# Optimization experiments

Measured on AMD Instinct MI355X. Metric: run time of the kernel, lower is better.

The kernel has to match this reference:

```python
import jax, jax.numpy as jnp
import numpy as np

B, C, H, W = 16, 64, 128, 128
BN_EPS = 1e-5


def setup_inputs() -> dict:
    key = jax.random.key(0)
    ks = jax.random.split(key, 8)
    inp = {
        "x1": jax.random.normal(ks[0], (B, C, H, W), dtype=jnp.float32),
        "x2": jax.random.normal(ks[1], (B, C, H, W), dtype=jnp.float32),
        "rssi1": jax.random.normal(ks[2], (B, C, H, W), dtype=jnp.float32),
        "rssi2": jax.random.normal(ks[3], (B, C, H, W), dtype=jnp.float32),
        # 1x1 conv weights == per-pixel channel matmul; trunc_normal(std=0.02) approximated by normal*0.02
        "q_w": jax.random.normal(ks[4], (C, C), dtype=jnp.float32) * 0.02,
        "q_b": jnp.zeros((C,), dtype=jnp.float32),
        "k_w": jax.random.normal(ks[5], (C, C), dtype=jnp.float32) * 0.02,
        "k_b": jnp.zeros((C,), dtype=jnp.float32),
        "v_w": jax.random.normal(ks[6], (C, C), dtype=jnp.float32) * 0.02,
        "v_b": jnp.zeros((C,), dtype=jnp.float32),
        "bn_gamma": jnp.ones((C,), dtype=jnp.float32),
        "bn_beta": jnp.zeros((C,), dtype=jnp.float32),
    }
    return inp


def _proj(w, b, x):
    # 1x1 Conv2d: contract channel dim
    return jnp.einsum('oc,bchw->bohw', w, x) + b[None, :, None, None]


def _branch(q_w, q_b, k_w, k_b, v_w, v_b, rssi, x):
    q = _proj(q_w, q_b, rssi)            # [B,C,H,W]
    k = _proj(k_w, k_b, x)               # [B,C,H,W]
    v = _proj(v_w, v_b, x)               # [B,C,H,W]
    scale = 1.0 / jnp.sqrt(jnp.asarray(k.shape[-2], dtype=q.dtype))
    # matmul over trailing dims: [B,C,H,W] @ [B,C,W,H] -> [B,C,H,H]
    score = jax.nn.softmax(jnp.einsum('bchw,bcgw->bchg', q, k) * scale, axis=-1)
    return jnp.einsum('bchg,bcgw->bchw', score, v)  # [B,C,H,W]


def reference(x1, x2, rssi1, rssi2, q_w, q_b, k_w, k_b, v_w, v_b, bn_gamma, bn_beta):
    csi1 = _branch(q_w, q_b, k_w, k_b, v_w, v_b, rssi1, x1)
    csi2 = _branch(q_w, q_b, k_w, k_b, v_w, v_b, rssi2, x2)
    fused = csi1 + csi2
    # BatchNorm2d (training mode -> batch statistics over B,H,W), then ReLU
    mean = jnp.mean(fused, axis=(0, 2, 3), keepdims=True)
    var = jnp.var(fused, axis=(0, 2, 3), keepdims=True)
    g = bn_gamma[None, :, None, None]
    b = bn_beta[None, :, None, None]
    normed = (fused - mean) * jax.lax.rsqrt(var + BN_EPS) * g + b
    return jax.nn.relu(normed)
```

## Files before the change

### kernel.cpp

```cpp
#include <hip/hip_runtime.h>

#define HW 16384
#define NE 16777216ull

typedef short bf16x8 __attribute__((ext_vector_type(8)));
typedef _Float16 f16x8 __attribute__((ext_vector_type(8)));
typedef float f32x4  __attribute__((ext_vector_type(4)));

__device__ __forceinline__ unsigned short f2bf(float f) {
    unsigned int u = __float_as_uint(f);
    unsigned int r = (u + 0x7FFFu + ((u >> 16) & 1u)) >> 16;
    return (unsigned short)r;
}
__device__ __forceinline__ float bf2f(unsigned short s) {
    return __uint_as_float(((unsigned int)s) << 16);
}

__global__ __launch_bounds__(128)
void zero_stats_kernel(float* __restrict__ stats) {
    stats[threadIdx.x] = 0.f;
}

__global__ __launch_bounds__(256)
void proj_mfma_kernel(const float* __restrict__ in,
                      const float* __restrict__ w1, const float* __restrict__ b1,
                      unsigned short* __restrict__ out1,
                      const float* __restrict__ w2, const float* __restrict__ b2,
                      unsigned short* __restrict__ out2) {
    __shared__ __align__(16) _Float16 xT[256 * 64];
    int tid = threadIdx.x;
    int pbase = blockIdx.x * 256;
    int b = pbase >> 14;
    int hw0 = pbase & 16383;
    const float* inb = in + (size_t)b * (64 * HW);

    {
        int n = tid;
        int swz = n & 7;
        const float* colp = inb + hw0 + n;
#pragma unroll
        for (int kc = 0; kc < 8; ++kc) {
            f16x8 ev;
#pragma unroll
            for (int j = 0; j < 8; ++j)
                ev[j] = (_Float16)colp[(kc * 8 + j) * HW];
            *reinterpret_cast<f16x8*>(&xT[n * 64 + ((kc ^ swz) * 8)]) = ev;
        }
    }

    int lane = tid & 63;
    int wv = tid >> 6;
    int quad = lane >> 4;
    int m16 = lane & 15;
    int mb = wv * 16;
    int sw = m16 & 7;
    int hasw2 = (w2 != nullptr);

    f16x8 a1[2], a2[2];
    float bias1[4], bias2[4];
#pragma unroll
    for (int ks = 0; ks < 2; ++ks) {
        const float* wr = w1 + (mb + m16) * 64 + (ks * 4 + quad) * 8;
        f16x8 ev;
#pragma unroll
        for (int j = 0; j < 8; ++j) ev[j] = (_Float16)wr[j];
        a1[ks] = ev;
    }
#pragma unroll
    for (int r = 0; r < 4; ++r) bias1[r] = b1[mb + quad * 4 + r];
    if (hasw2) {
#pragma unroll
        for (int ks = 0; ks < 2; ++ks) {
            const float* wr = w2 + (mb + m16) * 64 + (ks * 4 + quad) * 8;
            f16x8 ev;
#pragma unroll
            for (int j = 0; j < 8; ++j) ev[j] = (_Float16)wr[j];
            a2[ks] = ev;
        }
#pragma unroll
        for (int r = 0; r < 4; ++r) bias2[r] = b2[mb + quad * 4 + r];
    }
    __syncthreads();

    unsigned short* o1 = out1 + (size_t)b * (64 * HW);
    unsigned short* o2 = hasw2 ? (out2 + (size_t)b * (64 * HW)) : out1;

#pragma unroll
    for (int nt = 0; nt < 16; ++nt) {
        int row = nt * 16 + m16;
        f16x8 bF0 = *reinterpret_cast<const f16x8*>(&xT[row * 64 + ((quad ^ sw) * 8)]);
        f16x8 bF1 = *reinterpret_cast<const f16x8*>(&xT[row * 64 + (((4 + quad) ^ sw) * 8)]);
        f32x4 acc1 = {bias1[0], bias1[1], bias1[2], bias1[3]};
        acc1 = __builtin_amdgcn_mfma_f32_16x16x32_f16(a1[0], bF0, acc1, 0, 0, 0);
        acc1 = __builtin_amdgcn_mfma_f32_16x16x32_f16(a1[1], bF1, acc1, 0, 0, 0);
        int cbase = (mb + quad * 4) * HW + hw0 + nt * 16 + m16;
#pragma unroll
        for (int r = 0; r < 4; ++r)
            o1[cbase + r * HW] = f2bf(acc1[r]);
        if (hasw2) {
            f32x4 acc2 = {bias2[0], bias2[1], bias2[2], bias2[3]};
            acc2 = __builtin_amdgcn_mfma_f32_16x16x32_f16(a2[0], bF0, acc2, 0, 0, 0);
            acc2 = __builtin_amdgcn_mfma_f32_16x16x32_f16(a2[1], bF1, acc2, 0, 0, 0);
#pragma unroll
            for (int r = 0; r < 4; ++r)
                o2[cbase + r * HW] = f2bf(acc2[r]);
        }
    }
}

__global__ __launch_bounds__(512, 4)
void attn_kernel(const unsigned short* __restrict__ Q, const unsigned short* __restrict__ K,
                 const unsigned short* __restrict__ V, float* __restrict__ io,
                 float* __restrict__ stats, int accumulate) {
    __shared__ short bufA[16384];
    __shared__ short bufB[16384];
    int bc = blockIdx.x;
    size_t base = (size_t)bc * HW;
    int tid = threadIdx.x;
    int lane = tid & 63;
    int wv = tid >> 6;
    int quad = lane >> 4;
    int m16 = lane & 15;

    uint4 vreg[4];
    {
        int g0 = tid >> 4;
        int w0 = (tid & 15) * 8;
#pragma unroll
        for (int i = 0; i < 4; ++i)
            vreg[i] = *(const uint4*)(V + base + (size_t)(g0 + 32 * i) * 128 + w0);
    }

    {
        int r0 = tid >> 4;
        int c0 = tid & 15;
#pragma unroll
        for (int i = 0; i < 4; ++i) {
            int r = r0 + 32 * i;
            uint4 q = *(const uint4*)(Q + base + (size_t)r * 128 + c0 * 8);
            uint4 k = *(const uint4*)(K + base + (size_t)r * 128 + c0 * 8);
            int ch = c0 ^ (r & 7);
            *reinterpret_cast<uint4*>(&bufA[r * 128 + ch * 8]) = q;
            *reinterpret_cast<uint4*>(&bufB[r * 128 + ch * 8]) = k;
        }
    }
    __syncthreads();

    int rowA = wv * 16 + m16;
    int sw = m16 & 7;
    bf16x8 aF[4];
#pragma unroll
    for (int ks = 0; ks < 4; ++ks) {
        int ch = (ks * 4 + quad) ^ sw;
        aF[ks] = *reinterpret_cast<const bf16x8*>(&bufA[rowA * 128 + ch * 8]);
    }
    f32x4 sacc[8];
#pragma unroll
    for (int n = 0; n < 8; ++n) {
        f32x4 acc = {0.f, 0.f, 0.f, 0.f};
        int rowB = n * 16 + m16;
#pragma unroll
        for (int ks = 0; ks < 4; ++ks) {
            int ch = (ks * 4 + quad) ^ sw;
            bf16x8 bF = *reinterpret_cast<const bf16x8*>(&bufB[rowB * 128 + ch * 8]);
            acc = __builtin_amdgcn_mfma_f32_16x16x32_bf16(aF[ks], bF, acc, 0, 0, 0);
        }
        sacc[n] = acc;
    }

    const float scale = 0.08838834764831845f;
    float mx[4] = {-3.4e38f, -3.4e38f, -3.4e38f, -3.4e38f};
#pragma unroll
    for (int n = 0; n < 8; ++n)
#pragma unroll
        for (int r = 0; r < 4; ++r) {
            sacc[n][r] *= scale;
            mx[r] = fmaxf(mx[r], sacc[n][r]);
        }
#pragma unroll
    for (int mask = 8; mask >= 1; mask >>= 1)
#pragma unroll
        for (int r = 0; r < 4; ++r) mx[r] = fmaxf(mx[r], __shfl_xor(mx[r], mask));
    float sum[4] = {0.f, 0.f, 0.f, 0.f};
#pragma unroll
    for (int n = 0; n < 8; ++n)
#pragma unroll
        for (int r = 0; r < 4; ++r) {
            float e = __expf(sacc[n][r] - mx[r]);
            sacc[n][r] = e;
            sum[r] += e;
        }
#pragma unroll
    for (int mask = 8; mask >= 1; mask >>= 1)
#pragma unroll
        for (int r = 0; r < 4; ++r) sum[r] += __shfl_xor(sum[r], mask);
    float inv[4];
#pragma unroll
    for (int r = 0; r < 4; ++r) inv[r] = 1.0f / sum[r];

#pragma unroll
    for (int n = 0; n < 8; ++n)
#pragma unroll
        for (int r = 0; r < 4; ++r) {
            int row = wv * 16 + quad * 4 + r;
            int col = n * 16 + m16;
            int pos = row * 128 + (((col >> 3) ^ (row & 7)) * 8) + (col & 7);
            bufA[pos] = (short)f2bf(sacc[n][r] * inv[r]);
        }

    __syncthreads();

    {
        int g0 = tid >> 4;
        int w0 = (tid & 15) * 8;
#pragma unroll
        for (int i = 0; i < 4; ++i) {
            int g = g0 + 32 * i;
            unsigned short e[8];
            *(uint4*)e = vreg[i];
#pragma unroll
            for (int jj = 0; jj < 8; ++jj) {
                int j = jj ^ (tid & 7);
                int w = w0 + j;
                int pos = w * 128 + (((g >> 3) ^ (w & 7)) * 8) + (g & 7);
                bufB[pos] = (short)e[j];
            }
        }
    }
    __syncthreads();

#pragma unroll
    for (int ks = 0; ks < 4; ++ks) {
        int ch = (ks * 4 + quad) ^ sw;
        aF[ks] = *reinterpret_cast<const bf16x8*>(&bufA[rowA * 128 + ch * 8]);
    }
    f32x4 oacc[8];
#pragma unroll
    for (int n = 0; n < 8; ++n) {
        f32x4 acc = {0.f, 0.f, 0.f, 0.f};
        int rowB = n * 16 + m16;
#pragma unroll
        for (int ks = 0; ks < 4; ++ks) {
            int ch = (ks * 4 + quad) ^ sw;
            bf16x8 bF = *reinterpret_cast<const bf16x8*>(&bufB[rowB * 128 + ch * 8]);
            acc = __builtin_amdgcn_mfma_f32_16x16x32_bf16(aF[ks], bF, acc, 0, 0, 0);
        }
        oacc[n] = acc;
    }

    if (!accumulate) {
#pragma unroll
        for (int n = 0; n < 8; ++n)
#pragma unroll
            for (int r = 0; r < 4; ++r) {
                int row = wv * 16 + quad * 4 + r;
                int col = n * 16 + m16;
                io[base + row * 128 + col] = oacc[n][r];
            }
    } else {
        float lsum = 0.f, lsq = 0.f;
#pragma unroll
        for (int n = 0; n < 8; ++n)
#pragma unroll
            for (int r = 0; r < 4; ++r) {
                int row = wv * 16 + quad * 4 + r;
                int col = n * 16 + m16;
                size_t idx = base + row * 128 + col;
                float f = io[idx] + oacc[n][r];
                io[idx] = f;
                lsum += f;
                lsq += f * f;
            }
#pragma unroll
        for (int mask = 32; mask >= 1; mask >>= 1) {
            lsum += __shfl_xor(lsum, mask);
            lsq  += __shfl_xor(lsq,  mask);
        }
        if (lane == 0) {
            int c = bc & 63;
            atomicAdd(&stats[c], lsum);
            atomicAdd(&stats[64 + c], lsq);
        }
    }
}

__global__ __launch_bounds__(256)
void bn_relu_kernel(float* __restrict__ io, const float* __restrict__ stats,
                    const float* __restrict__ gamma, const float* __restrict__ beta) {
    int idx = blockIdx.x * 256 + threadIdx.x;
    int e = idx << 2;
    int c = (e >> 14) & 63;
    const float invN = 1.0f / 262144.0f;
    float mean = stats[c] * invN;
    float var = stats[64 + c] * invN - mean * mean;
    float k = rsqrtf(var + 1e-5f) * gamma[c];
    float bb = beta[c] - mean * k;
    float4 f = reinterpret_cast<const float4*>(io)[idx];
    float4 o;
    o.x = fmaxf(f.x * k + bb, 0.f);
    o.y = fmaxf(f.y * k + bb, 0.f);
    o.z = fmaxf(f.z * k + bb, 0.f);
    o.w = fmaxf(f.w * k + bb, 0.f);
    reinterpret_cast<float4*>(io)[idx] = o;
}

extern "C" void kernel_launch(void* const* d_in, const int* in_sizes, int n_in,
                              void* d_out, int out_size, void* d_ws, size_t ws_size,
                              hipStream_t stream) {
    const float* x1 = (const float*)d_in[0];
    const float* x2 = (const float*)d_in[1];
    const float* rssi1 = (const float*)d_in[2];
    const float* rssi2 = (const float*)d_in[3];
    const float* qw = (const float*)d_in[4];
    const float* qb = (const float*)d_in[5];
    const float* kw = (const float*)d_in[6];
    const float* kb = (const float*)d_in[7];
    const float* vw = (const float*)d_in[8];
    const float* vb = (const float*)d_in[9];
    const float* gamma = (const float*)d_in[10];
    const float* beta = (const float*)d_in[11];

    float* stats = (float*)d_ws;
    unsigned short* Q = (unsigned short*)((char*)d_ws + 512);
    unsigned short* K = Q + NE;
    unsigned short* V = K + NE;
    float* io = (float*)d_out;

    zero_stats_kernel<<<1, 128, 0, stream>>>(stats);

    proj_mfma_kernel<<<1024, 256, 0, stream>>>(rssi1, qw, qb, Q,
                                               nullptr, nullptr, nullptr);
    proj_mfma_kernel<<<1024, 256, 0, stream>>>(x1, kw, kb, K, vw, vb, V);
    attn_kernel<<<1024, 512, 0, stream>>>(Q, K, V, io, stats, 0);

    proj_mfma_kernel<<<1024, 256, 0, stream>>>(rssi2, qw, qb, Q,
                                               nullptr, nullptr, nullptr);
    proj_mfma_kernel<<<1024, 256, 0, stream>>>(x2, kw, kb, K, vw, vb, V);
    attn_kernel<<<1024, 512, 0, stream>>>(Q, K, V, io, stats, 1);

    bn_relu_kernel<<<16384, 256, 0, stream>>>(io, stats, gamma, beta);
}
```

Baseline: 451.3 us.

## Stage projection outputs through LDS for coalesced 16-byte stores; prefetch accumulator

The projection kernel now packs its bf16 results in registers, writes them into a swizzled shared-memory tile, and then stores each row with 16-byte vector writes. Before, each lane wrote scattered 2-byte stores. The stats zeroing moves into the first projection launch, which removes one kernel launch. The attention kernel also loads the previous io values early, before the V transpose, so that global load latency overlaps with other work. The cost is extra barriers, extra shared-memory traffic and higher register pressure (64 packed words plus 32 prefetched floats).

```diff
diff --git a/kernel.cpp b/kernel.cpp
--- a/kernel.cpp
+++ b/kernel.cpp
@@ -11,14 +11,6 @@
     unsigned int u = __float_as_uint(f);
     unsigned int r = (u + 0x7FFFu + ((u >> 16) & 1u)) >> 16;
     return (unsigned short)r;
-}
-__device__ __forceinline__ float bf2f(unsigned short s) {
-    return __uint_as_float(((unsigned int)s) << 16);
-}
-
-__global__ __launch_bounds__(128)
-void zero_stats_kernel(float* __restrict__ stats) {
-    stats[threadIdx.x] = 0.f;
 }
 
 __global__ __launch_bounds__(256)
@@ -26,9 +18,12 @@
                       const float* __restrict__ w1, const float* __restrict__ b1,
                       unsigned short* __restrict__ out1,
                       const float* __restrict__ w2, const float* __restrict__ b2,
-                      unsigned short* __restrict__ out2) {
+                      unsigned short* __restrict__ out2,
+                      float* __restrict__ stats) {
     __shared__ __align__(16) _Float16 xT[256 * 64];
+    unsigned short* obuf = reinterpret_cast<unsigned short*>(xT);
     int tid = threadIdx.x;
+    if (stats != nullptr && blockIdx.x == 0 && tid < 128) stats[tid] = 0.f;
     int pbase = blockIdx.x * 256;
     int b = pbase >> 14;
     int hw0 = pbase & 16383;
@@ -85,6 +80,7 @@
     unsigned short* o1 = out1 + (size_t)b * (64 * HW);
     unsigned short* o2 = hasw2 ? (out2 + (size_t)b * (64 * HW)) : out1;
 
+    unsigned int pk1[32], pk2[32];
 #pragma unroll
     for (int nt = 0; nt < 16; ++nt) {
         int row = nt * 16 + m16;
@@ -93,17 +89,58 @@
         f32x4 acc1 = {bias1[0], bias1[1], bias1[2], bias1[3]};
         acc1 = __builtin_amdgcn_mfma_f32_16x16x32_f16(a1[0], bF0, acc1, 0, 0, 0);
         acc1 = __builtin_amdgcn_mfma_f32_16x16x32_f16(a1[1], bF1, acc1, 0, 0, 0);
-        int cbase = (mb + quad * 4) * HW + hw0 + nt * 16 + m16;
-#pragma unroll
-        for (int r = 0; r < 4; ++r)
-            o1[cbase + r * HW] = f2bf(acc1[r]);
+        pk1[nt * 2 + 0] = (unsigned int)f2bf(acc1[0]) | ((unsigned int)f2bf(acc1[1]) << 16);
+        pk1[nt * 2 + 1] = (unsigned int)f2bf(acc1[2]) | ((unsigned int)f2bf(acc1[3]) << 16);
         if (hasw2) {
             f32x4 acc2 = {bias2[0], bias2[1], bias2[2], bias2[3]};
             acc2 = __builtin_amdgcn_mfma_f32_16x16x32_f16(a2[0], bF0, acc2, 0, 0, 0);
             acc2 = __builtin_amdgcn_mfma_f32_16x16x32_f16(a2[1], bF1, acc2, 0, 0, 0);
-#pragma unroll
-            for (int r = 0; r < 4; ++r)
-                o2[cbase + r * HW] = f2bf(acc2[r]);
+            pk2[nt * 2 + 0] = (unsigned int)f2bf(acc2[0]) | ((unsigned int)f2bf(acc2[1]) << 16);
+            pk2[nt * 2 + 1] = (unsigned int)f2bf(acc2[2]) | ((unsigned int)f2bf(acc2[3]) << 16);
+        }
+    }
+    __syncthreads();
+
+#pragma unroll
+    for (int nt = 0; nt < 16; ++nt)
+#pragma unroll
+        for (int r = 0; r < 4; ++r) {
+            int row = mb + quad * 4 + r;
+            int col = nt * 16 + m16;
+            unsigned int v = pk1[nt * 2 + (r >> 1)];
+            unsigned short e = (r & 1) ? (unsigned short)(v >> 16) : (unsigned short)(v & 0xffff);
+            obuf[row * 256 + (((col >> 3) ^ (row & 7)) * 8) + (col & 7)] = e;
+        }
+    __syncthreads();
+#pragma unroll
+    for (int k = 0; k < 8; ++k) {
+        int c = k * 256 + tid;
+        int row = c >> 5;
+        int cg = c & 31;
+        uint4 v = *reinterpret_cast<const uint4*>(&obuf[row * 256 + ((cg ^ (row & 7)) * 8)]);
+        *reinterpret_cast<uint4*>(&o1[(size_t)row * HW + hw0 + cg * 8]) = v;
+    }
+
+    if (hasw2) {
+        __syncthreads();
+#pragma unroll
+        for (int nt = 0; nt < 16; ++nt)
+#pragma unroll
+            for (int r = 0; r < 4; ++r) {
+                int row = mb + quad * 4 + r;
+                int col = nt * 16 + m16;
+                unsigned int v = pk2[nt * 2 + (r >> 1)];
+                unsigned short e = (r & 1) ? (unsigned short)(v >> 16) : (unsigned short)(v & 0xffff);
+                obuf[row * 256 + (((col >> 3) ^ (row & 7)) * 8) + (col & 7)] = e;
+            }
+        __syncthreads();
+#pragma unroll
+        for (int k = 0; k < 8; ++k) {
+            int c = k * 256 + tid;
+            int row = c >> 5;
+            int cg = c & 31;
+            uint4 v = *reinterpret_cast<const uint4*>(&obuf[row * 256 + ((cg ^ (row & 7)) * 8)]);
+            *reinterpret_cast<uint4*>(&o2[(size_t)row * HW + hw0 + cg * 8]) = v;
         }
     }
 }
@@ -210,6 +247,15 @@
 
     __syncthreads();
 
+    float iopre[8][4];
+    if (accumulate) {
+#pragma unroll
+        for (int n = 0; n < 8; ++n)
+#pragma unroll
+            for (int r = 0; r < 4; ++r)
+                iopre[n][r] = io[base + (wv * 16 + quad * 4 + r) * 128 + n * 16 + m16];
+    }
+
     {
         int g0 = tid >> 4;
         int w0 = (tid & 15) * 8;
@@ -266,7 +312,7 @@
                 int row = wv * 16 + quad * 4 + r;
                 int col = n * 16 + m16;
                 size_t idx = base + row * 128 + col;
-                float f = io[idx] + oacc[n][r];
+                float f = iopre[n][r] + oacc[n][r];
                 io[idx] = f;
                 lsum += f;
                 lsq += f * f;
@@ -326,16 +372,14 @@
     unsigned short* V = K + NE;
     float* io = (float*)d_out;
 
-    zero_stats_kernel<<<1, 128, 0, stream>>>(stats);
-
     proj_mfma_kernel<<<1024, 256, 0, stream>>>(rssi1, qw, qb, Q,
-                                               nullptr, nullptr, nullptr);
-    proj_mfma_kernel<<<1024, 256, 0, stream>>>(x1, kw, kb, K, vw, vb, V);
+                                               nullptr, nullptr, nullptr, stats);
+    proj_mfma_kernel<<<1024, 256, 0, stream>>>(x1, kw, kb, K, vw, vb, V, nullptr);
     attn_kernel<<<1024, 512, 0, stream>>>(Q, K, V, io, stats, 0);
 
     proj_mfma_kernel<<<1024, 256, 0, stream>>>(rssi2, qw, qb, Q,
-                                               nullptr, nullptr, nullptr);
-    proj_mfma_kernel<<<1024, 256, 0, stream>>>(x2, kw, kb, K, vw, vb, V);
+                                               nullptr, nullptr, nullptr, nullptr);
+    proj_mfma_kernel<<<1024, 256, 0, stream>>>(x2, kw, kb, K, vw, vb, V, nullptr);
     attn_kernel<<<1024, 512, 0, stream>>>(Q, K, V, io, stats, 1);
 
     bn_relu_kernel<<<16384, 256, 0, stream>>>(io, stats, gamma, beta);
```

Measured after the change: 443.5 us. No clear change (-1.7%).
